# Kernel tuning notes

Measured on AMD Instinct MI355X. Metric: run time of the kernel, lower is better.

Reference implementation:

```python
import jax, jax.numpy as jnp
import numpy as np

H = 8       # heads
D = 512     # hidden_size
DH = D // H # head dim
FF = 2048   # hardcoded FFN hidden in source


def _layernorm(x, g, b, eps=1e-5):
    mu = jnp.mean(x, axis=-1, keepdims=True)
    var = jnp.var(x, axis=-1, keepdims=True)
    return (x - mu) * jax.lax.rsqrt(var + eps) * g + b


def setup_inputs() -> dict:
    key = jax.random.key(0)
    ks = jax.random.split(key, 12)
    B, S = 2, 4096
    s = lambda fan_in: 1.0 / np.sqrt(fan_in)
    return {
        "reaction": jax.random.normal(ks[0], (B, S, D), dtype=jnp.float32),
        "mask": jnp.ones((B, 1, 1, S), dtype=jnp.int32),
        # attention weights stored as [in, out] (torch Linear weight.T)
        "Wq": jax.random.uniform(ks[1], (D, D), jnp.float32, -s(D), s(D)),
        "Wk": jax.random.uniform(ks[2], (D, D), jnp.float32, -s(D), s(D)),
        "Wv": jax.random.uniform(ks[3], (D, D), jnp.float32, -s(D), s(D)),
        "Wo": jax.random.uniform(ks[4], (D, D), jnp.float32, -s(D), s(D)),
        "bo": jnp.zeros((D,), jnp.float32),
        "W1": jax.random.uniform(ks[5], (D, FF), jnp.float32, -s(D), s(D)),
        "b1": jnp.zeros((FF,), jnp.float32),
        "W2": jax.random.uniform(ks[6], (FF, D), jnp.float32, -s(FF), s(FF)),
        "b2": jnp.zeros((D,), jnp.float32),
        "g_sa": jnp.ones((D,), jnp.float32),
        "b_sa": jnp.zeros((D,), jnp.float32),
        "g_ff": jnp.ones((D,), jnp.float32),
        "b_ff": jnp.zeros((D,), jnp.float32),
    }


def reference(reaction, mask, Wq, Wk, Wv, Wo, bo, W1, b1, W2, b2, g_sa, b_sa, g_ff, b_ff):
    B, S, _ = reaction.shape
    # --- self-attention part (pre-norm) ---
    x = _layernorm(reaction, g_sa, b_sa)
    q = (x @ Wq).reshape(B, S, H, DH)
    k = (x @ Wk).reshape(B, S, H, DH)
    v = (x @ Wv).reshape(B, S, H, DH)
    scale = DH ** (-0.5)
    scores = jnp.einsum('bqhd,bkhd->bhqk', q * scale, k)  # [B,H,S,S]
    scores = jnp.where(mask == 0, -jnp.inf, scores)
    att = jax.nn.softmax(scores, axis=-1)
    ctx = jnp.einsum('bhqk,bkhd->bqhd', att, v).reshape(B, S, D)
    attn_out = jax.nn.gelu(ctx @ Wo + bo, approximate=False)  # GELU after output proj (as in source)
    x = attn_out + reaction
    # --- feed-forward part (pre-norm) ---
    y = _layernorm(x, g_ff, b_ff)
    y = jax.nn.gelu(y @ W1 + b1, approximate=False) @ W2 + b2
    return y + x
```

## Files before the change

kernel.cpp:

```cpp
#include <hip/hip_runtime.h>
#include <hip/hip_bf16.h>
#include <math.h>

#define HN 8
#define DM 512
#define DHD 64
#define FFD 2048
#define BB 2
#define SS 4096
#define MT (BB*SS)

typedef __bf16 bf16_t;
typedef __bf16 bf16x8 __attribute__((ext_vector_type(8)));
typedef __bf16 bf16x4 __attribute__((ext_vector_type(4)));
typedef float  floatx4 __attribute__((ext_vector_type(4)));

__device__ __forceinline__ void async_copy16(const bf16_t* g, bf16_t* l) {
  __builtin_amdgcn_global_load_lds((const __attribute__((address_space(1))) void*)g,
                                   (__attribute__((address_space(3))) void*)l,
                                   16, 0, 0);
}

__device__ __forceinline__ float gelu_f(float x) {
  return 0.5f * x * (1.0f + erff(x * 0.70710678118654752f));
}

#if __has_builtin(__builtin_amdgcn_exp2f)
__device__ __forceinline__ float fast_exp2(float x) { return __builtin_amdgcn_exp2f(x); }
#else
__device__ __forceinline__ float fast_exp2(float x) { return __expf(x * 0.69314718056f); }
#endif

__global__ __launch_bounds__(256)
void ln_kernel(const float* __restrict__ x, const float* __restrict__ g,
               const float* __restrict__ be, bf16_t* __restrict__ out)
{
  const int row = blockIdx.x, t = threadIdx.x;
  const float* xr = x + (size_t)row * DM;
  float v0 = xr[t], v1 = xr[t + 256];
  float s = v0 + v1, s2 = v0 * v0 + v1 * v1;
#pragma unroll
  for (int o = 32; o > 0; o >>= 1) { s += __shfl_down(s, o); s2 += __shfl_down(s2, o); }
  __shared__ float red[8];
  if ((t & 63) == 0) { red[(t >> 6) * 2] = s; red[(t >> 6) * 2 + 1] = s2; }
  __syncthreads();
  float ts  = red[0] + red[2] + red[4] + red[6];
  float ts2 = red[1] + red[3] + red[5] + red[7];
  float mu = ts * (1.0f / DM);
  float rv = rsqrtf(ts2 * (1.0f / DM) - mu * mu + 1e-5f);
  out[(size_t)row * DM + t]       = (bf16_t)((v0 - mu) * rv * g[t]       + be[t]);
  out[(size_t)row * DM + t + 256] = (bf16_t)((v1 - mu) * rv * g[t + 256] + be[t + 256]);
}

__global__ __launch_bounds__(256)
void prep_weights(const float* __restrict__ Wq, const float* __restrict__ Wk,
                  const float* __restrict__ Wv, const float* __restrict__ Wo,
                  const float* __restrict__ W1, const float* __restrict__ W2,
                  bf16_t* __restrict__ WqkvT, bf16_t* __restrict__ WoT,
                  bf16_t* __restrict__ W1T, bf16_t* __restrict__ W2T)
{
  const int bid = blockIdx.x;
  const float* src; bf16_t* dst; int Kd, Nd, n0, k0;
  if (bid < 768) {
    int seg = bid >> 8, t = bid & 255;
    src = (seg == 0) ? Wq : (seg == 1) ? Wk : Wv;
    dst = WqkvT + (size_t)seg * 512 * 512;
    Kd = 512; Nd = 512; n0 = (t & 15) * 32; k0 = (t >> 4) * 32;
  } else if (bid < 1024) {
    int t = bid - 768; src = Wo; dst = WoT;
    Kd = 512; Nd = 512; n0 = (t & 15) * 32; k0 = (t >> 4) * 32;
  } else if (bid < 2048) {
    int t = bid - 1024; src = W1; dst = W1T;
    Kd = 512; Nd = 2048; n0 = (t & 63) * 32; k0 = (t >> 6) * 32;
  } else {
    int t = bid - 2048; src = W2; dst = W2T;
    Kd = 2048; Nd = 512; n0 = (t & 15) * 32; k0 = (t >> 4) * 32;
  }
  __shared__ float tile[32][33];
  const int tx = threadIdx.x & 31, ty = threadIdx.x >> 5;
#pragma unroll
  for (int i = 0; i < 32; i += 8)
    tile[ty + i][tx] = src[(size_t)(k0 + ty + i) * Nd + n0 + tx];
  __syncthreads();
#pragma unroll
  for (int i = 0; i < 32; i += 8)
    dst[(size_t)(n0 + ty + i) * Kd + k0 + tx] = (bf16_t)tile[tx][ty + i];
}

template <int MI, int NJ, int EPI>
__global__ __launch_bounds__(256)
void gemm_bt(const bf16_t* __restrict__ A, const bf16_t* __restrict__ Bt,
             const int M, const int N, const int K,
             const float* __restrict__ bias, const float* __restrict__ res,
             bf16_t* __restrict__ outb, float* __restrict__ outf,
             bf16_t* __restrict__ out2, bf16_t* __restrict__ out3, const int ldt)
{
  constexpr int MTILE = 32 * MI, NTILE = 32 * NJ;
  constexpr int ACOPY = MTILE / 32;
  constexpr int BCOPY = NTILE / 32;
  __shared__ __align__(16) bf16_t lA[MTILE * 64];
  __shared__ __align__(16) bf16_t lB[NTILE * 64];
  const int tid = threadIdx.x;
  const int wave = tid >> 6, lane = tid & 63;
  const int wm = wave & 1, wn = wave >> 1;
  const int quad = lane >> 4, l16 = lane & 15;

  int srA[ACOPY > BCOPY ? ACOPY : BCOPY], scA[ACOPY > BCOPY ? ACOPY : BCOPY];
#pragma unroll
  for (int i = 0; i < (ACOPY > BCOPY ? ACOPY : BCOPY); ++i) {
    int flat = tid + 256 * i;
    int r = flat >> 3, ch = flat & 7;
    srA[i] = r;
    scA[i] = (ch ^ (r & 7)) * 8;
  }
  const bf16_t* Ab = A + (size_t)(blockIdx.x * MTILE) * K;
  const bf16_t* Bb = Bt + (size_t)(blockIdx.y * NTILE) * K;

  const floatx4 vzero = {0.f, 0.f, 0.f, 0.f};
  floatx4 acc[MI][NJ];
#pragma unroll
  for (int i = 0; i < MI; ++i)
#pragma unroll
    for (int j = 0; j < NJ; ++j) acc[i][j] = vzero;

  for (int k0 = 0; k0 < K; k0 += 64) {
    __syncthreads();
#pragma unroll
    for (int i = 0; i < ACOPY; ++i)
      async_copy16(Ab + (size_t)srA[i] * K + k0 + scA[i], lA + (tid + 256 * i) * 8);
#pragma unroll
    for (int i = 0; i < BCOPY; ++i)
      async_copy16(Bb + (size_t)srA[i] * K + k0 + scA[i], lB + (tid + 256 * i) * 8);
    __syncthreads();
#pragma unroll
    for (int c = 0; c < 2; ++c) {
      bf16x8 af[MI], bfv[NJ];
#pragma unroll
      for (int i = 0; i < MI; ++i)
        af[i] = *(const bf16x8*)(lA + (wm * 16 * MI + i * 16 + l16) * 64
                                 + (((c * 4 + quad) ^ (l16 & 7)) * 8));
#pragma unroll
      for (int j = 0; j < NJ; ++j)
        bfv[j] = *(const bf16x8*)(lB + (wn * 16 * NJ + j * 16 + l16) * 64
                                  + (((c * 4 + quad) ^ (l16 & 7)) * 8));
#pragma unroll
      for (int i = 0; i < MI; ++i)
#pragma unroll
        for (int j = 0; j < NJ; ++j)
          acc[i][j] = __builtin_amdgcn_mfma_f32_16x16x32_bf16(af[i], bfv[j], acc[i][j], 0, 0, 0);
    }
  }

  const int m00 = blockIdx.x * MTILE + wm * 16 * MI;
  const int n00 = blockIdx.y * NTILE + wn * 16 * NJ;
#pragma unroll
  for (int i = 0; i < MI; ++i) {
#pragma unroll
    for (int j = 0; j < NJ; ++j) {
      const int m0 = m00 + i * 16 + quad * 4;
      const int n  = n00 + j * 16 + l16;
      floatx4 v = acc[i][j];
      if (EPI == 2) {
        const float bb = bias[n];
#pragma unroll
        for (int r = 0; r < 4; ++r)
          outf[(size_t)(m0 + r) * N + n] = gelu_f(v[r] + bb) + res[(size_t)(m0 + r) * N + n];
      } else if (EPI == 3) {
        const float bb = bias[n];
#pragma unroll
        for (int r = 0; r < 4; ++r)
          outb[(size_t)(m0 + r) * N + n] = (bf16_t)gelu_f(v[r] + bb);
      } else if (EPI == 4) {
        const float bb = bias[n];
#pragma unroll
        for (int r = 0; r < 4; ++r)
          outf[(size_t)(m0 + r) * N + n] = v[r] + bb + res[(size_t)(m0 + r) * N + n];
      } else {
        const int seg = blockIdx.y >> 2;
        if (seg == 0) {
#pragma unroll
          for (int r = 0; r < 4; ++r)
            outb[(size_t)(m0 + r) * 512 + n] = (bf16_t)(v[r] * 0.180336879f);
        } else if (seg == 1) {
#pragma unroll
          for (int r = 0; r < 4; ++r) out2[(size_t)(m0 + r) * 512 + (n - 512)] = (bf16_t)v[r];
        } else {
          bf16x4 pk = {(bf16_t)v[0], (bf16_t)v[1], (bf16_t)v[2], (bf16_t)v[3]};
          *(bf16x4*)(out3 + (size_t)(n - 1024) * ldt + m0) = pk;
        }
      }
    }
  }
}

__global__ __launch_bounds__(256, 4)
void attn_kernel(const bf16_t* __restrict__ qm, const bf16_t* __restrict__ km,
                 const bf16_t* __restrict__ vtm, const int* __restrict__ mask,
                 bf16_t* __restrict__ ctx)
{
  const int b = blockIdx.z, h = blockIdx.y;
  const int q0 = blockIdx.x * 64;
  const int tid = threadIdx.x;
  const int wave = tid >> 6, lane = tid & 63;
  const int quad = lane >> 4, l16 = lane & 15;

  __shared__ __align__(16) bf16_t lK[128 * DHD];
  __shared__ __align__(16) bf16_t lV[DHD * 128];
  __shared__ int sclean[4];

  const int* maskb = mask + b * SS;

  unsigned um = 0xFFFFFFFFu;
#pragma unroll
  for (int i = 0; i < 4; ++i) {
    int4 m = *(const int4*)(maskb + tid * 16 + i * 4);
    um = min(um, min(min((unsigned)m.x, (unsigned)m.y), min((unsigned)m.z, (unsigned)m.w)));
  }
#pragma unroll
  for (int o = 1; o < 64; o <<= 1) um = min(um, (unsigned)__shfl_xor((int)um, o));
  if (lane == 0) sclean[wave] = (int)um;
  __syncthreads();
  const bool clean = (min(min((unsigned)sclean[0], (unsigned)sclean[1]),
                          min((unsigned)sclean[2], (unsigned)sclean[3])) != 0u);

  const size_t qrow0 = (size_t)b * SS + q0;
  bf16x8 qa[2];
#pragma unroll
  for (int c = 0; c < 2; ++c)
    qa[c] = *(const bf16x8*)(qm + (qrow0 + wave * 16 + l16) * DM
                             + h * DHD + c * 32 + quad * 8);

  bf16x8 vone8;
#pragma unroll
  for (int t = 0; t < 8; ++t) vone8[t] = (bf16_t)1.0f;

  const floatx4 vzero = {0.f, 0.f, 0.f, 0.f};
  floatx4 cacc[4], lacc;
  lacc = vzero;
#pragma unroll
  for (int nb = 0; nb < 4; ++nb) cacc[nb] = vzero;

  const bf16_t* Kb = km + (size_t)b * SS * DM + h * DHD;
  const bf16_t* Vb = vtm + (size_t)(h * DHD) * MT + (size_t)b * SS;

  for (int s0 = 0; s0 < SS; s0 += 128) {
    __syncthreads();
#pragma unroll
    for (int i = 0; i < 4; ++i) {
      int p = tid + 256 * i;
      int key = p >> 3;
      int cs = (p & 7) ^ (key & 7);
      async_copy16(Kb + (size_t)(s0 + key) * DM + cs * 8, lK + p * 8);
      int dh = p >> 4;
      int cs2 = (p & 15) ^ (dh & 7);
      async_copy16(Vb + (size_t)dh * MT + s0 + cs2 * 8, lV + p * 8);
    }
    __syncthreads();

#pragma unroll
    for (int c = 0; c < 4; ++c) {
      floatx4 sa = vzero, sb = vzero;
#pragma unroll
      for (int cc = 0; cc < 2; ++cc) {
        const int ko = ((cc * 4 + quad) ^ (l16 & 7)) * 8;
        bf16x8 kf0 = *(const bf16x8*)(lK + (c * 32 + l16) * 64 + ko);
        bf16x8 kf1 = *(const bf16x8*)(lK + (c * 32 + 16 + l16) * 64 + ko);
        sa = __builtin_amdgcn_mfma_f32_16x16x32_bf16(kf0, qa[cc], sa, 0, 0, 0);
        sb = __builtin_amdgcn_mfma_f32_16x16x32_bf16(kf1, qa[cc], sb, 0, 0, 0);
      }

      if (!clean) {
        const int4 m0 = *(const int4*)(maskb + s0 + c * 32 + quad * 4);
        const int4 m1 = *(const int4*)(maskb + s0 + c * 32 + 16 + quad * 4);
        if (m0.x == 0) sa[0] = -1e30f;
        if (m0.y == 0) sa[1] = -1e30f;
        if (m0.z == 0) sa[2] = -1e30f;
        if (m0.w == 0) sa[3] = -1e30f;
        if (m1.x == 0) sb[0] = -1e30f;
        if (m1.y == 0) sb[1] = -1e30f;
        if (m1.z == 0) sb[2] = -1e30f;
        if (m1.w == 0) sb[3] = -1e30f;
      }

      bf16x8 pf;
      pf[0] = (bf16_t)fast_exp2(sa[0]); pf[1] = (bf16_t)fast_exp2(sa[1]);
      pf[2] = (bf16_t)fast_exp2(sa[2]); pf[3] = (bf16_t)fast_exp2(sa[3]);
      pf[4] = (bf16_t)fast_exp2(sb[0]); pf[5] = (bf16_t)fast_exp2(sb[1]);
      pf[6] = (bf16_t)fast_exp2(sb[2]); pf[7] = (bf16_t)fast_exp2(sb[3]);

      lacc = __builtin_amdgcn_mfma_f32_16x16x32_bf16(vone8, pf, lacc, 0, 0, 0);
      const int ch_lo = (4 * c + (quad >> 1)) ^ (l16 & 7);
#pragma unroll
      for (int nb = 0; nb < 4; ++nb) {
        const bf16_t* base = lV + (nb * 16 + l16) * 128 + (quad & 1) * 4;
        bf16x4 vlo = *(const bf16x4*)(base + ch_lo * 8);
        bf16x4 vhi = *(const bf16x4*)(base + (ch_lo ^ 2) * 8);
        bf16x8 av = __builtin_shufflevector(vlo, vhi, 0, 1, 2, 3, 4, 5, 6, 7);
        cacc[nb] = __builtin_amdgcn_mfma_f32_16x16x32_bf16(av, pf, cacc[nb], 0, 0, 0);
      }
    }
  }

  const float inv = 1.0f / lacc[0];
  const size_t qrow = qrow0 + wave * 16 + l16;
#pragma unroll
  for (int nb = 0; nb < 4; ++nb) {
    bf16x4 o = {(bf16_t)(cacc[nb][0] * inv), (bf16_t)(cacc[nb][1] * inv),
                (bf16_t)(cacc[nb][2] * inv), (bf16_t)(cacc[nb][3] * inv)};
    *(bf16x4*)(ctx + qrow * DM + h * DHD + nb * 16 + quad * 4) = o;
  }
}

extern "C" void kernel_launch(void* const* d_in, const int* in_sizes, int n_in,
                              void* d_out, int out_size, void* d_ws, size_t ws_size,
                              hipStream_t stream)
{
  (void)in_sizes; (void)n_in; (void)out_size; (void)ws_size;
  const float* reaction = (const float*)d_in[0];
  const int*   mask     = (const int*)d_in[1];
  const float* Wq = (const float*)d_in[2];
  const float* Wk = (const float*)d_in[3];
  const float* Wv = (const float*)d_in[4];
  const float* Wo = (const float*)d_in[5];
  const float* bo = (const float*)d_in[6];
  const float* W1 = (const float*)d_in[7];
  const float* b1 = (const float*)d_in[8];
  const float* W2 = (const float*)d_in[9];
  const float* b2 = (const float*)d_in[10];
  const float* g_sa = (const float*)d_in[11];
  const float* b_sa = (const float*)d_in[12];
  const float* g_ff = (const float*)d_in[13];
  const float* b_ff = (const float*)d_in[14];
  float* out = (float*)d_out;

  char* ws = (char*)d_ws;
  size_t off = 0;
  auto take = [&](size_t bytes) -> char* {
    char* p = ws + off;
    off += (bytes + 255) & ~(size_t)255;
    return p;
  };

  bf16_t* xln   = (bf16_t*)take((size_t)MT * DM * 2);
  bf16_t* WqkvT = (bf16_t*)take((size_t)3 * DM * DM * 2);
  bf16_t* WoT   = (bf16_t*)take((size_t)DM * DM * 2);
  bf16_t* W1T   = (bf16_t*)take((size_t)FFD * DM * 2);
  bf16_t* W2T   = (bf16_t*)take((size_t)DM * FFD * 2);
  bf16_t* qb    = (bf16_t*)take((size_t)MT * DM * 2);
  bf16_t* kb    = (bf16_t*)take((size_t)MT * DM * 2);
  bf16_t* vtb   = (bf16_t*)take((size_t)DM * MT * 2);
  bf16_t* ctx   = (bf16_t*)take((size_t)MT * DM * 2);
  float*  x2    = (float*)take((size_t)MT * DM * 4);
  bf16_t* yb    = xln;
  bf16_t* hb    = qb;

  ln_kernel<<<MT, 256, 0, stream>>>(reaction, g_sa, b_sa, xln);
  prep_weights<<<3072, 256, 0, stream>>>(Wq, Wk, Wv, Wo, W1, W2, WqkvT, WoT, W1T, W2T);

  gemm_bt<4, 4, 5><<<dim3(64, 12), 256, 0, stream>>>(xln, WqkvT, MT, 3 * DM, DM,
                                                     nullptr, nullptr, qb, nullptr, kb, vtb, MT);

  attn_kernel<<<dim3(SS / 64, HN, BB), 256, 0, stream>>>(qb, kb, vtb, mask, ctx);

  gemm_bt<2, 2, 2><<<dim3(128, 8), 256, 0, stream>>>(ctx, WoT, MT, DM, DM,
                                                     bo, reaction, nullptr, x2, nullptr, nullptr, 0);

  ln_kernel<<<MT, 256, 0, stream>>>(x2, g_ff, b_ff, yb);
  gemm_bt<4, 4, 3><<<dim3(64, 16), 256, 0, stream>>>(yb, W1T, MT, FFD, DM,
                                                     b1, nullptr, hb, nullptr, nullptr, nullptr, 0);
  gemm_bt<2, 2, 4><<<dim3(128, 8), 256, 0, stream>>>(hb, W2T, MT, DM, FFD,
                                                     b2, x2, nullptr, out, nullptr, nullptr, 0);
}
```

Baseline: 306.0 us.

## Load K fragments directly to registers and pre-permute V^T for single LDS reads

```diff
diff --git a/kernel.cpp b/kernel.cpp
--- a/kernel.cpp
+++ b/kernel.cpp
@@ -185,8 +185,10 @@
 #pragma unroll
           for (int r = 0; r < 4; ++r) out2[(size_t)(m0 + r) * 512 + (n - 512)] = (bf16_t)v[r];
         } else {
+          const int o = m0 & 31;
+          const int p0 = (m0 & ~31) + ((o >> 2) & 3) * 8 + ((o >> 4) << 2);
           bf16x4 pk = {(bf16_t)v[0], (bf16_t)v[1], (bf16_t)v[2], (bf16_t)v[3]};
-          *(bf16x4*)(out3 + (size_t)(n - 1024) * ldt + m0) = pk;
+          *(bf16x4*)(out3 + (size_t)(n - 1024) * ldt + p0) = pk;
         }
       }
     }
@@ -204,7 +206,6 @@
   const int wave = tid >> 6, lane = tid & 63;
   const int quad = lane >> 4, l16 = lane & 15;
 
-  __shared__ __align__(16) bf16_t lK[128 * DHD];
   __shared__ __align__(16) bf16_t lV[DHD * 128];
   __shared__ int sclean[4];
 
@@ -240,20 +241,25 @@
 #pragma unroll
   for (int nb = 0; nb < 4; ++nb) cacc[nb] = vzero;
 
-  const bf16_t* Kb = km + (size_t)b * SS * DM + h * DHD;
+  const bf16_t* Kf = km + ((size_t)b * SS + l16) * DM + h * DHD + quad * 8;
   const bf16_t* Vb = vtm + (size_t)(h * DHD) * MT + (size_t)b * SS;
 
   for (int s0 = 0; s0 < SS; s0 += 128) {
     __syncthreads();
+    bf16x8 kf[4][2][2];
+#pragma unroll
+    for (int c = 0; c < 4; ++c)
+#pragma unroll
+      for (int hf = 0; hf < 2; ++hf)
+#pragma unroll
+        for (int cc = 0; cc < 2; ++cc)
+          kf[c][hf][cc] = *(const bf16x8*)(Kf + (size_t)(s0 + c * 32 + hf * 16) * DM + cc * 32);
 #pragma unroll
     for (int i = 0; i < 4; ++i) {
       int p = tid + 256 * i;
-      int key = p >> 3;
-      int cs = (p & 7) ^ (key & 7);
-      async_copy16(Kb + (size_t)(s0 + key) * DM + cs * 8, lK + p * 8);
       int dh = p >> 4;
-      int cs2 = (p & 15) ^ (dh & 7);
-      async_copy16(Vb + (size_t)dh * MT + s0 + cs2 * 8, lV + p * 8);
+      int cs = (p & 15) ^ (dh & 7);
+      async_copy16(Vb + (size_t)dh * MT + s0 + cs * 8, lV + p * 8);
     }
     __syncthreads();
 
@@ -262,11 +268,8 @@
       floatx4 sa = vzero, sb = vzero;
 #pragma unroll
       for (int cc = 0; cc < 2; ++cc) {
-        const int ko = ((cc * 4 + quad) ^ (l16 & 7)) * 8;
-        bf16x8 kf0 = *(const bf16x8*)(lK + (c * 32 + l16) * 64 + ko);
-        bf16x8 kf1 = *(const bf16x8*)(lK + (c * 32 + 16 + l16) * 64 + ko);
-        sa = __builtin_amdgcn_mfma_f32_16x16x32_bf16(kf0, qa[cc], sa, 0, 0, 0);
-        sb = __builtin_amdgcn_mfma_f32_16x16x32_bf16(kf1, qa[cc], sb, 0, 0, 0);
+        sa = __builtin_amdgcn_mfma_f32_16x16x32_bf16(kf[c][0][cc], qa[cc], sa, 0, 0, 0);
+        sb = __builtin_amdgcn_mfma_f32_16x16x32_bf16(kf[c][1][cc], qa[cc], sb, 0, 0, 0);
       }
 
       if (!clean) {
@@ -289,13 +292,10 @@
       pf[6] = (bf16_t)fast_exp2(sb[2]); pf[7] = (bf16_t)fast_exp2(sb[3]);
 
       lacc = __builtin_amdgcn_mfma_f32_16x16x32_bf16(vone8, pf, lacc, 0, 0, 0);
-      const int ch_lo = (4 * c + (quad >> 1)) ^ (l16 & 7);
+      const int ch = (c * 4 + quad) ^ (l16 & 7);
 #pragma unroll
       for (int nb = 0; nb < 4; ++nb) {
-        const bf16_t* base = lV + (nb * 16 + l16) * 128 + (quad & 1) * 4;
-        bf16x4 vlo = *(const bf16x4*)(base + ch_lo * 8);
-        bf16x4 vhi = *(const bf16x4*)(base + (ch_lo ^ 2) * 8);
-        bf16x8 av = __builtin_shufflevector(vlo, vhi, 0, 1, 2, 3, 4, 5, 6, 7);
+        bf16x8 av = *(const bf16x8*)(lV + (nb * 16 + l16) * 128 + ch * 8);
         cacc[nb] = __builtin_amdgcn_mfma_f32_16x16x32_bf16(av, pf, cacc[nb], 0, 0, 0);
       }
     }
```

Result: slower. 462.2 us (+51.0%).

## Double query rows per attention block and pre-permute V layout for single LDS loads

Applied to the files above, without the earlier changes.

```diff
diff --git a/kernel.cpp b/kernel.cpp
--- a/kernel.cpp
+++ b/kernel.cpp
@@ -185,21 +185,23 @@
 #pragma unroll
           for (int r = 0; r < 4; ++r) out2[(size_t)(m0 + r) * 512 + (n - 512)] = (bf16_t)v[r];
         } else {
+          const int o = m0 & 31;
+          const int p0 = (m0 & ~31) + ((o >> 2) & 3) * 8 + ((o >> 4) << 2);
           bf16x4 pk = {(bf16_t)v[0], (bf16_t)v[1], (bf16_t)v[2], (bf16_t)v[3]};
-          *(bf16x4*)(out3 + (size_t)(n - 1024) * ldt + m0) = pk;
+          *(bf16x4*)(out3 + (size_t)(n - 1024) * ldt + p0) = pk;
         }
       }
     }
   }
 }
 
-__global__ __launch_bounds__(256, 4)
+__global__ __launch_bounds__(256, 2)
 void attn_kernel(const bf16_t* __restrict__ qm, const bf16_t* __restrict__ km,
                  const bf16_t* __restrict__ vtm, const int* __restrict__ mask,
                  bf16_t* __restrict__ ctx)
 {
   const int b = blockIdx.z, h = blockIdx.y;
-  const int q0 = blockIdx.x * 64;
+  const int q0 = blockIdx.x * 128;
   const int tid = threadIdx.x;
   const int wave = tid >> 6, lane = tid & 63;
   const int quad = lane >> 4, l16 = lane & 15;
@@ -224,21 +226,26 @@
                           min((unsigned)sclean[2], (unsigned)sclean[3])) != 0u);
 
   const size_t qrow0 = (size_t)b * SS + q0;
-  bf16x8 qa[2];
-#pragma unroll
-  for (int c = 0; c < 2; ++c)
-    qa[c] = *(const bf16x8*)(qm + (qrow0 + wave * 16 + l16) * DM
-                             + h * DHD + c * 32 + quad * 8);
+  bf16x8 qa[2][2];
+#pragma unroll
+  for (int mb = 0; mb < 2; ++mb)
+#pragma unroll
+    for (int cc = 0; cc < 2; ++cc)
+      qa[mb][cc] = *(const bf16x8*)(qm + (qrow0 + wave * 32 + mb * 16 + l16) * DM
+                                    + h * DHD + cc * 32 + quad * 8);
 
   bf16x8 vone8;
 #pragma unroll
   for (int t = 0; t < 8; ++t) vone8[t] = (bf16_t)1.0f;
 
   const floatx4 vzero = {0.f, 0.f, 0.f, 0.f};
-  floatx4 cacc[4], lacc;
-  lacc = vzero;
-#pragma unroll
-  for (int nb = 0; nb < 4; ++nb) cacc[nb] = vzero;
+  floatx4 cacc[2][4], lacc[2];
+#pragma unroll
+  for (int mb = 0; mb < 2; ++mb) {
+    lacc[mb] = vzero;
+#pragma unroll
+    for (int nb = 0; nb < 4; ++nb) cacc[mb][nb] = vzero;
+  }
 
   const bf16_t* Kb = km + (size_t)b * SS * DM + h * DHD;
   const bf16_t* Vb = vtm + (size_t)(h * DHD) * MT + (size_t)b * SS;
@@ -259,55 +266,65 @@
 
 #pragma unroll
     for (int c = 0; c < 4; ++c) {
-      floatx4 sa = vzero, sb = vzero;
+      floatx4 sa[2], sb[2];
+      sa[0] = vzero; sa[1] = vzero; sb[0] = vzero; sb[1] = vzero;
 #pragma unroll
       for (int cc = 0; cc < 2; ++cc) {
         const int ko = ((cc * 4 + quad) ^ (l16 & 7)) * 8;
         bf16x8 kf0 = *(const bf16x8*)(lK + (c * 32 + l16) * 64 + ko);
         bf16x8 kf1 = *(const bf16x8*)(lK + (c * 32 + 16 + l16) * 64 + ko);
-        sa = __builtin_amdgcn_mfma_f32_16x16x32_bf16(kf0, qa[cc], sa, 0, 0, 0);
-        sb = __builtin_amdgcn_mfma_f32_16x16x32_bf16(kf1, qa[cc], sb, 0, 0, 0);
+#pragma unroll
+        for (int mb = 0; mb < 2; ++mb) {
+          sa[mb] = __builtin_amdgcn_mfma_f32_16x16x32_bf16(kf0, qa[mb][cc], sa[mb], 0, 0, 0);
+          sb[mb] = __builtin_amdgcn_mfma_f32_16x16x32_bf16(kf1, qa[mb][cc], sb[mb], 0, 0, 0);
+        }
       }
 
       if (!clean) {
         const int4 m0 = *(const int4*)(maskb + s0 + c * 32 + quad * 4);
         const int4 m1 = *(const int4*)(maskb + s0 + c * 32 + 16 + quad * 4);
-        if (m0.x == 0) sa[0] = -1e30f;
-        if (m0.y == 0) sa[1] = -1e30f;
-        if (m0.z == 0) sa[2] = -1e30f;
-        if (m0.w == 0) sa[3] = -1e30f;
-        if (m1.x == 0) sb[0] = -1e30f;
-        if (m1.y == 0) sb[1] = -1e30f;
-        if (m1.z == 0) sb[2] = -1e30f;
-        if (m1.w == 0) sb[3] = -1e30f;
-      }
-
-      bf16x8 pf;
-      pf[0] = (bf16_t)fast_exp2(sa[0]); pf[1] = (bf16_t)fast_exp2(sa[1]);
-      pf[2] = (bf16_t)fast_exp2(sa[2]); pf[3] = (bf16_t)fast_exp2(sa[3]);
-      pf[4] = (bf16_t)fast_exp2(sb[0]); pf[5] = (bf16_t)fast_exp2(sb[1]);
-      pf[6] = (bf16_t)fast_exp2(sb[2]); pf[7] = (bf16_t)fast_exp2(sb[3]);
-
-      lacc = __builtin_amdgcn_mfma_f32_16x16x32_bf16(vone8, pf, lacc, 0, 0, 0);
-      const int ch_lo = (4 * c + (quad >> 1)) ^ (l16 & 7);
+#pragma unroll
+        for (int mb = 0; mb < 2; ++mb) {
+          if (m0.x == 0) sa[mb][0] = -1e30f;
+          if (m0.y == 0) sa[mb][1] = -1e30f;
+          if (m0.z == 0) sa[mb][2] = -1e30f;
+          if (m0.w == 0) sa[mb][3] = -1e30f;
+          if (m1.x == 0) sb[mb][0] = -1e30f;
+          if (m1.y == 0) sb[mb][1] = -1e30f;
+          if (m1.z == 0) sb[mb][2] = -1e30f;
+          if (m1.w == 0) sb[mb][3] = -1e30f;
+        }
+      }
+
+      bf16x8 pf[2];
+#pragma unroll
+      for (int mb = 0; mb < 2; ++mb) {
+        pf[mb][0] = (bf16_t)fast_exp2(sa[mb][0]); pf[mb][1] = (bf16_t)fast_exp2(sa[mb][1]);
+        pf[mb][2] = (bf16_t)fast_exp2(sa[mb][2]); pf[mb][3] = (bf16_t)fast_exp2(sa[mb][3]);
+        pf[mb][4] = (bf16_t)fast_exp2(sb[mb][0]); pf[mb][5] = (bf16_t)fast_exp2(sb[mb][1]);
+        pf[mb][6] = (bf16_t)fast_exp2(sb[mb][2]); pf[mb][7] = (bf16_t)fast_exp2(sb[mb][3]);
+        lacc[mb] = __builtin_amdgcn_mfma_f32_16x16x32_bf16(vone8, pf[mb], lacc[mb], 0, 0, 0);
+      }
+      const int ch = (c * 4 + quad) ^ (l16 & 7);
 #pragma unroll
       for (int nb = 0; nb < 4; ++nb) {
-        const bf16_t* base = lV + (nb * 16 + l16) * 128 + (quad & 1) * 4;
-        bf16x4 vlo = *(const bf16x4*)(base + ch_lo * 8);
-        bf16x4 vhi = *(const bf16x4*)(base + (ch_lo ^ 2) * 8);
-        bf16x8 av = __builtin_shufflevector(vlo, vhi, 0, 1, 2, 3, 4, 5, 6, 7);
-        cacc[nb] = __builtin_amdgcn_mfma_f32_16x16x32_bf16(av, pf, cacc[nb], 0, 0, 0);
-      }
-    }
-  }
-
-  const float inv = 1.0f / lacc[0];
-  const size_t qrow = qrow0 + wave * 16 + l16;
-#pragma unroll
-  for (int nb = 0; nb < 4; ++nb) {
-    bf16x4 o = {(bf16_t)(cacc[nb][0] * inv), (bf16_t)(cacc[nb][1] * inv),
-                (bf16_t)(cacc[nb][2] * inv), (bf16_t)(cacc[nb][3] * inv)};
-    *(bf16x4*)(ctx + qrow * DM + h * DHD + nb * 16 + quad * 4) = o;
+        bf16x8 av = *(const bf16x8*)(lV + (nb * 16 + l16) * 128 + ch * 8);
+        cacc[0][nb] = __builtin_amdgcn_mfma_f32_16x16x32_bf16(av, pf[0], cacc[0][nb], 0, 0, 0);
+        cacc[1][nb] = __builtin_amdgcn_mfma_f32_16x16x32_bf16(av, pf[1], cacc[1][nb], 0, 0, 0);
+      }
+    }
+  }
+
+#pragma unroll
+  for (int mb = 0; mb < 2; ++mb) {
+    const float inv = 1.0f / lacc[mb][0];
+    const size_t qrow = qrow0 + wave * 32 + mb * 16 + l16;
+#pragma unroll
+    for (int nb = 0; nb < 4; ++nb) {
+      bf16x4 o = {(bf16_t)(cacc[mb][nb][0] * inv), (bf16_t)(cacc[mb][nb][1] * inv),
+                  (bf16_t)(cacc[mb][nb][2] * inv), (bf16_t)(cacc[mb][nb][3] * inv)};
+      *(bf16x4*)(ctx + qrow * DM + h * DHD + nb * 16 + quad * 4) = o;
+    }
   }
 }
 
@@ -360,7 +377,7 @@
   gemm_bt<4, 4, 5><<<dim3(64, 12), 256, 0, stream>>>(xln, WqkvT, MT, 3 * DM, DM,
                                                      nullptr, nullptr, qb, nullptr, kb, vtb, MT);
 
-  attn_kernel<<<dim3(SS / 64, HN, BB), 256, 0, stream>>>(qb, kb, vtb, mask, ctx);
+  attn_kernel<<<dim3(SS / 128, HN, BB), 256, 0, stream>>>(qb, kb, vtb, mask, ctx);
 
   gemm_bt<2, 2, 2><<<dim3(128, 8), 256, 0, stream>>>(ctx, WoT, MT, DM, DM,
                                                      bo, reaction, nullptr, x2, nullptr, nullptr, 0);
```

Result: faster. 283.3 us (-7.4%).
